# Optimization experiments

Hardware: AMD Instinct MI355X
Metric: run time of the kernel (lower is better)

Reference implementation:

```python
import jax, jax.numpy as jnp
import numpy as np

T, B, I, H = 512, 256, 512, 512


def setup_inputs() -> dict:
    key = jax.random.key(0)
    ks = jax.random.split(key, 10)
    inp = {
        "x": jax.random.normal(ks[0], (T, B, I), dtype=jnp.float32),
        "lengths": jax.random.randint(ks[1], (B,), 1, T + 1).astype(jnp.int64),
        # LSTMCell params, gate order [i, f, g, o]; forget-gate bias init to 1
        "W_ih": jax.random.normal(ks[2], (4 * H, I), dtype=jnp.float32) / np.sqrt(I),
        "W_hh": jax.random.normal(ks[3], (4 * H, H), dtype=jnp.float32) / np.sqrt(H),
        "b_ih": jnp.zeros((4 * H,), jnp.float32).at[H:2 * H].set(1.0),
        "b_hh": jnp.zeros((4 * H,), jnp.float32),
        # multiplicative projections
        "mx_w": jax.random.normal(ks[4], (H, I), dtype=jnp.float32) / np.sqrt(I),
        "mx_b": jnp.zeros((H,), jnp.float32),
        "mh_w": jax.random.normal(ks[5], (H, H), dtype=jnp.float32) / np.sqrt(H),
        "mh_b": jnp.zeros((H,), jnp.float32),
        "h0": jnp.zeros((H,), jnp.float32),
        "c0": jnp.zeros((H,), jnp.float32),
    }
    return inp


def _mlstm(x, lengths, W_ih, W_hh, b_ih, b_hh, mx_w, mx_b, mh_w, mh_b, h0, c0):
    Tn, Bn, _ = x.shape
    Hn = h0.shape[0]
    # Precompute all input-side projections in two big GEMMs (batched over T*B).
    xg = jnp.einsum('tbi,gi->tbg', x, W_ih) + b_ih          # [T,B,4H]
    xm = jnp.einsum('tbi,hi->tbh', x, mx_w) + mx_b          # [T,B,H]
    # active[t,b] = t < lengths[b]; padded steps freeze (h,c) -> packed semantics
    active = (jnp.arange(Tn)[:, None] < lengths[None, :])[..., None]  # [T,B,1]

    def step(carry, inp):
        h, c = carry
        xg_t, xm_t, act = inp
        m = xm_t * (h @ mh_w.T + mh_b)                       # multiplicative hidden
        gates = xg_t + m @ W_hh.T + b_hh                     # cell(x, (m, c))
        i, f, g, o = jnp.split(gates, 4, axis=-1)
        c_new = jax.nn.sigmoid(f) * c + jax.nn.sigmoid(i) * jnp.tanh(g)
        h_new = jax.nn.sigmoid(o) * jnp.tanh(c_new)
        h = jnp.where(act, h_new, h)
        c = jnp.where(act, c_new, c)
        return (h, c), None

    h_init = jnp.broadcast_to(h0, (Bn, Hn))
    c_init = jnp.broadcast_to(c0, (Bn, Hn))
    (h, c), _ = jax.lax.scan(step, (h_init, c_init), (xg, xm, active))
    # Torch code returns final cell state of each sequence, in batch order.
    return c


def reference(x, lengths, W_ih, W_hh, b_ih, b_hh, mx_w, mx_b, mh_w, mh_b, h0, c0):
    return _mlstm(x, lengths, W_ih, W_hh, b_ih, b_hh, mx_w, mx_b, mh_w, mh_b, h0, c0)
```

## Files before the change

kernel.cpp:

```cpp
#include <hip/hip_runtime.h>
#include <stdint.h>


typedef __attribute__((ext_vector_type(8))) short s8v;
typedef __attribute__((ext_vector_type(8))) _Float16 h8v;
typedef __attribute__((ext_vector_type(4))) float f4v;

#define SC 2048.0f
#define ISC (1.0f / 2048.0f)

__device__ __forceinline__ f4v mf(s8v a, s8v b, f4v c) {
  return __builtin_amdgcn_mfma_f32_16x16x32_f16(
      __builtin_bit_cast(h8v, a), __builtin_bit_cast(h8v, b), c, 0, 0, 0);
}
__device__ __forceinline__ uint16_t f2h(float x) {
  _Float16 h = (_Float16)x;
  return __builtin_bit_cast(uint16_t, h);
}
__device__ __forceinline__ void split2(float v, uint16_t& hi, uint16_t& lo) {
  _Float16 h = (_Float16)v;
  float r = v - (float)h;
  hi = __builtin_bit_cast(uint16_t, h);
  lo = f2h(r * SC);
}
__device__ __forceinline__ float sigm(float x) { return 1.0f / (1.0f + __expf(-x)); }
__device__ __forceinline__ float tanh_f(float x) { return 1.0f - 2.0f / (__expf(2.0f * x) + 1.0f); }

__device__ __forceinline__ s8v ldx4_sc1(const uint16_t* p) {
  s8v r;
  asm volatile("global_load_dwordx4 %0, %1, off sc1" : "=v"(r) : "v"(p));
  return r;
}
__device__ __forceinline__ uint32_t ld32_sc1(const uint32_t* p) {
  uint32_t r;
  asm volatile("global_load_dword %0, %1, off sc1" : "=v"(r) : "v"(p));
  return r;
}
__device__ __forceinline__ void st16_sc1(uint16_t* p, uint32_t v) {
  asm volatile("global_store_short %0, %1, off sc1" ::"v"(p), "v"(v) : "memory");
}
__device__ __forceinline__ void st32_sc1(uint32_t* p, uint32_t v) {
  asm volatile("global_store_dword %0, %1, off sc1" ::"v"(p), "v"(v) : "memory");
}

__global__ __launch_bounds__(256) void k_split(const float* __restrict__ x,
                                               uint16_t* __restrict__ xh,
                                               uint16_t* __restrict__ xl, long n) {
  long i = ((long)blockIdx.x * 256 + threadIdx.x) * 8;
  if (i >= n) return;
  float4 a = *(const float4*)(x + i);
  float4 b = *(const float4*)(x + i + 4);
  union { uint16_t u[8]; s8v v; } oh, ol;
  float vv[8] = {a.x, a.y, a.z, a.w, b.x, b.y, b.z, b.w};
#pragma unroll
  for (int k = 0; k < 8; ++k) split2(vv[k], oh.u[k], ol.u[k]);
  *(s8v*)(xh + i) = oh.v;
  *(s8v*)(xl + i) = ol.v;
}

__global__ __launch_bounds__(64) void k_packw(const float* __restrict__ Wg,
                                              const float* __restrict__ Wm,
                                              uint16_t* __restrict__ wh,
                                              uint16_t* __restrict__ wl) {
  int s = blockIdx.x >> 4, kt = blockIdx.x & 15, l = threadIdx.x;
  const float* src = (s < 128) ? (Wg + (size_t)(s * 16 + (l & 15)) * 512)
                               : (Wm + (size_t)((s - 128) * 16 + (l & 15)) * 512);
  int k0 = kt * 32 + (l >> 4) * 8;
  float4 a = *(const float4*)(src + k0);
  float4 b = *(const float4*)(src + k0 + 4);
  union { uint16_t u[8]; s8v v; } oh, ol;
  float vv[8] = {a.x, a.y, a.z, a.w, b.x, b.y, b.z, b.w};
#pragma unroll
  for (int k = 0; k < 8; ++k) split2(vv[k], oh.u[k], ol.u[k]);
  size_t adr = ((size_t)(s * 16 + kt) * 64 + l) * 8;
  *(s8v*)(wh + adr) = oh.v;
  *(s8v*)(wl + adr) = ol.v;
}

__device__ __forceinline__ void gpass(const uint16_t* __restrict__ Ap,
                                      const uint16_t* __restrict__ Bp,
                                      s8v* Asm, s8v* Bsm, int rowbase, int s0,
                                      f4v (&acc)[4][4]) {
  int tid = threadIdx.x;
  int wv = tid >> 6, l = tid & 63, wm = wv >> 1, wn = wv & 1;
  int arow = tid >> 1, ahalf = tid & 1, swz = (arow & 7) << 4;
  for (int ks = 0; ks < 8; ++ks) {
    __syncthreads();
    const uint16_t* asrc = Ap + (size_t)(rowbase + arow) * 512 + ks * 64;
#pragma unroll
    for (int q = 0; q < 4; ++q) {
      int pb = ahalf * 64 + q * 16;
      Asm[arow * 8 + (pb >> 4)] = *(const s8v*)(asrc + ((pb ^ swz) >> 1));
    }
#pragma unroll
    for (int q = 0; q < 4; ++q) {
      int ofs = tid * 64 + q * 16;
      int si = ofs >> 11, kti = (ofs >> 10) & 1, inner = ofs & 1023;
      Bsm[ofs >> 4] =
          *(const s8v*)(Bp + (size_t)((s0 + si) * 16 + ks * 2 + kti) * 512 + (inner >> 1));
    }
    __syncthreads();
#pragma unroll
    for (int kti = 0; kti < 2; ++kti) {
      s8v a[4], b[4];
#pragma unroll
      for (int i = 0; i < 4; ++i) {
        int row = wm * 64 + i * 16 + (l & 15);
        int lb = kti * 64 + (l >> 4) * 16;
        a[i] = Asm[row * 8 + ((lb ^ ((l & 7) << 4)) >> 4)];
      }
#pragma unroll
      for (int jj = 0; jj < 4; ++jj) b[jj] = Bsm[((wn * 4 + jj) * 2 + kti) * 64 + l];
#pragma unroll
      for (int i = 0; i < 4; ++i)
#pragma unroll
        for (int jj = 0; jj < 4; ++jj) acc[i][jj] = mf(a[i], b[jj], acc[i][jj]);
    }
  }
}

__global__ __launch_bounds__(256, 2) void k_gemm3(const uint16_t* __restrict__ xh,
                                                  const uint16_t* __restrict__ xl,
                                                  const uint16_t* __restrict__ wh,
                                                  const uint16_t* __restrict__ wl,
                                                  float* __restrict__ blob, int row0) {
  __shared__ s8v Asm[1024], Bsm[1024];
  f4v acc_a[4][4], acc_c[4][4];
#pragma unroll
  for (int i = 0; i < 4; ++i)
#pragma unroll
    for (int jj = 0; jj < 4; ++jj) {
      acc_a[i][jj] = (f4v){0.f, 0.f, 0.f, 0.f};
      acc_c[i][jj] = (f4v){0.f, 0.f, 0.f, 0.f};
    }
  int s0 = blockIdx.x * 8, r0 = blockIdx.y * 128;
  int rowbase = row0 + r0;
  gpass(xh, wh, Asm, Bsm, rowbase, s0, acc_a);
  gpass(xh, wl, Asm, Bsm, rowbase, s0, acc_c);
  gpass(xl, wh, Asm, Bsm, rowbase, s0, acc_c);
  int tid = threadIdx.x, wv = tid >> 6, l = tid & 63, wm = wv >> 1, wn = wv & 1;
#pragma unroll
  for (int i = 0; i < 4; ++i)
#pragma unroll
    for (int jj = 0; jj < 4; ++jj) {
      int s = s0 + wn * 4 + jj;
#pragma unroll
      for (int ri = 0; ri < 4; ++ri) {
        int trow = r0 + wm * 64 + i * 16 + (l >> 4) * 4 + ri;
        int tt = trow >> 8, gg = (trow >> 5) & 7, rr = trow & 31;
        size_t adr = ((size_t)(tt * 160 + s) * 8 + gg) * 512 + rr * 16 + (l & 15);
        blob[adr] = acc_a[i][jj][ri] + acc_c[i][jj][ri] * ISC;
      }
    }
}

__device__ __forceinline__ void gbar(uint32_t* slots, int myslot, uint32_t ep) {
  asm volatile("s_waitcnt vmcnt(0)" ::: "memory");
  __syncthreads();
  int tid = threadIdx.x;
  if (tid == 0) st32_sc1(slots + myslot, ep);
  if (tid < 64) {
    uint32_t v;
    const uint32_t* q = slots + (tid & 31);
    do {
      __builtin_amdgcn_s_sleep(1);
      v = ld32_sc1(q);
      asm volatile("s_waitcnt vmcnt(0)" ::: "memory");
      __builtin_amdgcn_sched_barrier(0);
    } while (!__all(v >= ep));
  }
  __syncthreads();
}

__global__ __launch_bounds__(128, 1) void k_rec(
    const uint16_t* __restrict__ wrh, const uint16_t* __restrict__ wrl,
    const float* __restrict__ blob,
    const float* __restrict__ b_ih, const float* __restrict__ b_hh,
    const float* __restrict__ mx_b, const float* __restrict__ mh_b,
    const float* __restrict__ h0, const float* __restrict__ c0,
    const int* __restrict__ lengths,
    uint16_t* hh, uint16_t* hl, uint16_t* mhp, uint16_t* mlp,
    float* cbuf, uint32_t* flags, float* out, int chunk) {
  extern __shared__ char smraw[];
  s8v* SW = (s8v*)smraw;
  int tid = threadIdx.x, l = tid & 63, mt = tid >> 6;
  int g = blockIdx.x & 7, j = blockIdx.x >> 3;

  for (int p = 0; p < 2; ++p) {
    const uint16_t* wp = p ? wrl : wrh;
    for (int nt = 0; nt < 4; ++nt) {
      const s8v* src = (const s8v*)(wp + (size_t)(nt * 32 + j) * 8192);
#pragma unroll
      for (int it = 0; it < 8; ++it) SW[p * 4096 + nt * 1024 + it * 128 + tid] = src[it * 128 + tid];
    }
  }
  s8v wmh[16], wml[16];
  {
    const s8v* sH = (const s8v*)(wrh + (size_t)(128 + j) * 8192);
    const s8v* sL = (const s8v*)(wrl + (size_t)(128 + j) * 8192);
#pragma unroll
    for (int kt = 0; kt < 16; ++kt) { wmh[kt] = sH[kt * 64 + l]; wml[kt] = sL[kt * 64 + l]; }
  }
  int cidx = l & 15, rq = l >> 4;
  int hc = j * 16 + cidx;
  float mhb = mh_b[hc], mxb = mx_b[hc];
  float bsum[4];
#pragma unroll
  for (int nt = 0; nt < 4; ++nt) bsum[nt] = b_ih[nt * 512 + hc] + b_hh[nt * 512 + hc];
  int rowA = g * 32 + mt * 16 + cidx;
  int kofs = rq * 8;
  int rowC0 = g * 32 + mt * 16 + rq * 4;
  float creg[4];
  int lenr[4];
#pragma unroll
  for (int ri = 0; ri < 4; ++ri) {
    int r = rowC0 + ri;
    lenr[ri] = lengths[r];
    creg[ri] = (chunk == 0) ? c0[hc] : cbuf[(size_t)r * 512 + hc];
  }
  if (chunk == 0) {
    uint16_t hi, lo;
    split2(h0[hc], hi, lo);
#pragma unroll
    for (int ri = 0; ri < 4; ++ri) {
      st16_sc1(hh + (size_t)(rowC0 + ri) * 512 + hc, hi);
      st16_sc1(hl + (size_t)(rowC0 + ri) * 512 + hc, lo);
    }
  }
  uint32_t* slots = flags + g * 64;
  uint32_t ep = 1;
  gbar(slots, j, ep);

  const uint16_t* hrb = hh + (size_t)rowA * 512 + kofs;
  const uint16_t* lrb = hl + (size_t)rowA * 512 + kofs;
  const uint16_t* mrb = mhp + (size_t)rowA * 512 + kofs;
  const uint16_t* nrb = mlp + (size_t)rowA * 512 + kofs;

  for (int t = 0; t < 128; ++t) {
    size_t bb = ((size_t)(t * 160 + j) * 8 + g) * 512 + (size_t)(mt * 16 + rq * 4) * 16 + cidx;
    float bxm[4], bg[4][4];
#pragma unroll
    for (int ri = 0; ri < 4; ++ri) {
      bxm[ri] = blob[bb + 524288 + ri * 16];
#pragma unroll
      for (int nt = 0; nt < 4; ++nt) bg[nt][ri] = blob[bb + nt * 131072 + ri * 16];
    }
    s8v ah[16], al[16];
#pragma unroll
    for (int kt = 0; kt < 16; ++kt) {
      ah[kt] = ldx4_sc1(hrb + kt * 32);
      al[kt] = ldx4_sc1(lrb + kt * 32);
    }
    asm volatile("s_waitcnt vmcnt(0)" ::: "memory");
    __builtin_amdgcn_sched_barrier(0);
    f4v a1a0 = (f4v){0,0,0,0}, a1a1 = (f4v){0,0,0,0}, a1c0 = (f4v){0,0,0,0}, a1c1 = (f4v){0,0,0,0};
#pragma unroll
    for (int kt = 0; kt < 16; kt += 2) {
      a1a0 = mf(ah[kt], wmh[kt], a1a0);
      a1a1 = mf(ah[kt + 1], wmh[kt + 1], a1a1);
    }
#pragma unroll
    for (int kt = 0; kt < 16; ++kt) {
      a1c0 = mf(ah[kt], wml[kt], a1c0);
      a1c1 = mf(al[kt], wmh[kt], a1c1);
    }
#pragma unroll
    for (int ri = 0; ri < 4; ++ri) {
      float hv = a1a0[ri] + a1a1[ri] + (a1c0[ri] + a1c1[ri]) * ISC + mhb;
      float mv = (bxm[ri] + mxb) * hv;
      uint16_t hi, lo;
      split2(mv, hi, lo);
      st16_sc1(mhp + (size_t)(rowC0 + ri) * 512 + hc, hi);
      st16_sc1(mlp + (size_t)(rowC0 + ri) * 512 + hc, lo);
    }
    ++ep;
    gbar(slots, j, ep);
#pragma unroll
    for (int kt = 0; kt < 16; ++kt) {
      ah[kt] = ldx4_sc1(mrb + kt * 32);
      al[kt] = ldx4_sc1(nrb + kt * 32);
    }
    asm volatile("s_waitcnt vmcnt(0)" ::: "memory");
    __builtin_amdgcn_sched_barrier(0);
    f4v p2a[4], p2c[4];
#pragma unroll
    for (int nt = 0; nt < 4; ++nt) { p2a[nt] = (f4v){0,0,0,0}; p2c[nt] = (f4v){0,0,0,0}; }
#pragma unroll
    for (int kt = 0; kt < 16; ++kt)
#pragma unroll
      for (int nt = 0; nt < 4; ++nt) p2a[nt] = mf(ah[kt], SW[nt * 1024 + kt * 64 + l], p2a[nt]);
#pragma unroll
    for (int kt = 0; kt < 16; ++kt)
#pragma unroll
      for (int nt = 0; nt < 4; ++nt) {
        p2c[nt] = mf(ah[kt], SW[4096 + nt * 1024 + kt * 64 + l], p2c[nt]);
        p2c[nt] = mf(al[kt], SW[nt * 1024 + kt * 64 + l], p2c[nt]);
      }
#pragma unroll
    for (int ri = 0; ri < 4; ++ri) {
      float gi = p2a[0][ri] + p2c[0][ri] * ISC + bsum[0] + bg[0][ri];
      float gf = p2a[1][ri] + p2c[1][ri] * ISC + bsum[1] + bg[1][ri];
      float gc = p2a[2][ri] + p2c[2][ri] * ISC + bsum[2] + bg[2][ri];
      float go = p2a[3][ri] + p2c[3][ri] * ISC + bsum[3] + bg[3][ri];
      float iv = sigm(gi), fv = sigm(gf), gv = tanh_f(gc), ov = sigm(go);
      float cn = fv * creg[ri] + iv * gv;
      float hn = ov * tanh_f(cn);
      bool act = (chunk * 128 + t) < lenr[ri];
      if (act) {
        creg[ri] = cn;
        uint16_t hi, lo;
        split2(hn, hi, lo);
        st16_sc1(hh + (size_t)(rowC0 + ri) * 512 + hc, hi);
        st16_sc1(hl + (size_t)(rowC0 + ri) * 512 + hc, lo);
      }
    }
    ++ep;
    gbar(slots, j, ep);
  }
#pragma unroll
  for (int ri = 0; ri < 4; ++ri) {
    cbuf[(size_t)(rowC0 + ri) * 512 + hc] = creg[ri];
    if (chunk == 3) out[(size_t)(rowC0 + ri) * 512 + hc] = creg[ri];
  }
}

extern "C" void kernel_launch(void* const* d_in, const int* in_sizes, int n_in,
                              void* d_out, int out_size, void* d_ws, size_t ws_size,
                              hipStream_t stream) {
  (void)in_sizes; (void)n_in; (void)out_size;
  const float* x = (const float*)d_in[0];
  const int* lengths = (const int*)d_in[1];
  const float* W_ih = (const float*)d_in[2];
  const float* W_hh = (const float*)d_in[3];
  const float* b_ih = (const float*)d_in[4];
  const float* b_hh = (const float*)d_in[5];
  const float* mx_w = (const float*)d_in[6];
  const float* mx_b = (const float*)d_in[7];
  const float* mh_w = (const float*)d_in[8];
  const float* mh_b = (const float*)d_in[9];
  const float* h0 = (const float*)d_in[10];
  const float* c0 = (const float*)d_in[11];

  if (ws_size < 616040448ull) return;

  char* ws = (char*)d_ws;
  uint16_t* xh = (uint16_t*)(ws);
  uint16_t* xl = (uint16_t*)(ws + 134217728ull);
  uint16_t* wpre_h = (uint16_t*)(ws + 268435456ull);
  uint16_t* wpre_l = (uint16_t*)(ws + 271056896ull);
  uint16_t* wrec_h = (uint16_t*)(ws + 273678336ull);
  uint16_t* wrec_l = (uint16_t*)(ws + 276299776ull);
  float* blob = (float*)(ws + 278921216ull);
  uint16_t* hh = (uint16_t*)(ws + 614465536ull);
  uint16_t* hl = (uint16_t*)(ws + 614727680ull);
  uint16_t* mhp = (uint16_t*)(ws + 614989824ull);
  uint16_t* mlp = (uint16_t*)(ws + 615251968ull);
  float* cbuf = (float*)(ws + 615514112ull);
  uint32_t* flags = (uint32_t*)(ws + 616038400ull);

  k_split<<<32768, 256, 0, stream>>>(x, xh, xl, 67108864L);
  k_packw<<<2560, 64, 0, stream>>>(W_ih, mx_w, wpre_h, wpre_l);
  k_packw<<<2560, 64, 0, stream>>>(W_hh, mh_w, wrec_h, wrec_l);
  hipFuncSetAttribute(reinterpret_cast<const void*>(k_rec),
                      hipFuncAttributeMaxDynamicSharedMemorySize, 131072);
  for (int c = 0; c < 4; ++c) {
    k_gemm3<<<dim3(20, 256), 256, 0, stream>>>(xh, xl, wpre_h, wpre_l, blob, c * 32768);
    hipMemsetAsync(flags, 0, 2048, stream);
    k_rec<<<256, 128, 131072, stream>>>(wrec_h, wrec_l, blob, b_ih, b_hh, mx_b, mh_b,
                                        h0, c0, lengths, hh, hl, mhp, mlp, cbuf,
                                        flags, (float*)d_out, c);
  }
}
```

Measured before the change: 8.768 ms.

## Replace block-wide grid barriers with per-wave flag polling over 16-row groups

Each wave now owns a 16-row batch group and synchronises only with the 32 waves sharing that group through separate m and h flag arrays, instead of a block-wide __syncthreads plus 32-slot barrier. The blob layout is reindexed to the finer 16-row grouping, and the h-ready flag is published at the end of a step but polled only after the next step's blob loads, letting those loads overlap the wait. Register pressure is cut by moving the low mh weights into LDS, which grows shared memory to 144 KiB, and by loading high and low activation fragments in sequence. The cost is more flag traffic and serialised load-then-MFMA phases with extra vmcnt waits.

After: 8.448 ms. -3.6%, faster.

```diff
diff --git a/kernel.cpp b/kernel.cpp
--- a/kernel.cpp
+++ b/kernel.cpp
@@ -42,6 +42,11 @@
 __device__ __forceinline__ void st32_sc1(uint32_t* p, uint32_t v) {
   asm volatile("global_store_dword %0, %1, off sc1" ::"v"(p), "v"(v) : "memory");
 }
+#define VM0                                              \
+  do {                                                   \
+    asm volatile("s_waitcnt vmcnt(0)" ::: "memory");     \
+    __builtin_amdgcn_sched_barrier(0);                   \
+  } while (0)
 
 __global__ __launch_bounds__(256) void k_split(const float* __restrict__ x,
                                                uint16_t* __restrict__ xh,
@@ -147,29 +152,21 @@
 #pragma unroll
       for (int ri = 0; ri < 4; ++ri) {
         int trow = r0 + wm * 64 + i * 16 + (l >> 4) * 4 + ri;
-        int tt = trow >> 8, gg = (trow >> 5) & 7, rr = trow & 31;
-        size_t adr = ((size_t)(tt * 160 + s) * 8 + gg) * 512 + rr * 16 + (l & 15);
+        int tt = trow >> 8, gg = (trow >> 4) & 15, rr = trow & 15;
+        size_t adr = ((size_t)(tt * 160 + s) * 16 + gg) * 256 + rr * 16 + (l & 15);
         blob[adr] = acc_a[i][jj][ri] + acc_c[i][jj][ri] * ISC;
       }
     }
 }
 
-__device__ __forceinline__ void gbar(uint32_t* slots, int myslot, uint32_t ep) {
-  asm volatile("s_waitcnt vmcnt(0)" ::: "memory");
-  __syncthreads();
-  int tid = threadIdx.x;
-  if (tid == 0) st32_sc1(slots + myslot, ep);
-  if (tid < 64) {
-    uint32_t v;
-    const uint32_t* q = slots + (tid & 31);
-    do {
-      __builtin_amdgcn_s_sleep(1);
-      v = ld32_sc1(q);
-      asm volatile("s_waitcnt vmcnt(0)" ::: "memory");
-      __builtin_amdgcn_sched_barrier(0);
-    } while (!__all(v >= ep));
-  }
-  __syncthreads();
+__device__ __forceinline__ void spoll(const uint32_t* slots, uint32_t ep, int l) {
+  const uint32_t* q = slots + (l & 31);
+  for (;;) {
+    uint32_t v = ld32_sc1(q);
+    VM0;
+    if (__all((int)(v >= ep))) break;
+    __builtin_amdgcn_s_sleep(1);
+  }
 }
 
 __global__ __launch_bounds__(128, 1) void k_rec(
@@ -183,33 +180,33 @@
     float* cbuf, uint32_t* flags, float* out, int chunk) {
   extern __shared__ char smraw[];
   s8v* SW = (s8v*)smraw;
-  int tid = threadIdx.x, l = tid & 63, mt = tid >> 6;
-  int g = blockIdx.x & 7, j = blockIdx.x >> 3;
-
-  for (int p = 0; p < 2; ++p) {
-    const uint16_t* wp = p ? wrl : wrh;
-    for (int nt = 0; nt < 4; ++nt) {
-      const s8v* src = (const s8v*)(wp + (size_t)(nt * 32 + j) * 8192);
-#pragma unroll
-      for (int it = 0; it < 8; ++it) SW[p * 4096 + nt * 1024 + it * 128 + tid] = src[it * 128 + tid];
-    }
-  }
-  s8v wmh[16], wml[16];
+  int tid = threadIdx.x, l = tid & 63, wv = tid >> 6;
+  int j = blockIdx.x >> 3, gg = ((blockIdx.x & 7) << 1) | wv;
+
+#pragma unroll
+  for (int sl = 0; sl < 9; ++sl) {
+    int gs = (sl < 4) ? (sl * 32 + j) : (sl < 8 ? (sl - 4) * 32 + j : 128 + j);
+    const s8v* src = (const s8v*)(((sl < 4) ? wrh : wrl) + (size_t)gs * 8192);
+#pragma unroll
+    for (int it = 0; it < 8; ++it) SW[sl * 1024 + it * 128 + tid] = src[it * 128 + tid];
+  }
+  s8v wmh[16];
   {
     const s8v* sH = (const s8v*)(wrh + (size_t)(128 + j) * 8192);
-    const s8v* sL = (const s8v*)(wrl + (size_t)(128 + j) * 8192);
-#pragma unroll
-    for (int kt = 0; kt < 16; ++kt) { wmh[kt] = sH[kt * 64 + l]; wml[kt] = sL[kt * 64 + l]; }
-  }
+#pragma unroll
+    for (int kt = 0; kt < 16; ++kt) wmh[kt] = sH[kt * 64 + l];
+  }
+  __syncthreads();
+
   int cidx = l & 15, rq = l >> 4;
   int hc = j * 16 + cidx;
   float mhb = mh_b[hc], mxb = mx_b[hc];
   float bsum[4];
 #pragma unroll
   for (int nt = 0; nt < 4; ++nt) bsum[nt] = b_ih[nt * 512 + hc] + b_hh[nt * 512 + hc];
-  int rowA = g * 32 + mt * 16 + cidx;
+  int rowA = gg * 16 + cidx;
   int kofs = rq * 8;
-  int rowC0 = g * 32 + mt * 16 + rq * 4;
+  int rowC0 = gg * 16 + rq * 4;
   float creg[4];
   int lenr[4];
 #pragma unroll
@@ -218,6 +215,9 @@
     lenr[ri] = lengths[r];
     creg[ri] = (chunk == 0) ? c0[hc] : cbuf[(size_t)r * 512 + hc];
   }
+  uint32_t* mslot = flags + gg * 32;
+  uint32_t* hslot = flags + 512 + gg * 32;
+
   if (chunk == 0) {
     uint16_t hi, lo;
     split2(h0[hc], hi, lo);
@@ -227,9 +227,9 @@
       st16_sc1(hl + (size_t)(rowC0 + ri) * 512 + hc, lo);
     }
   }
-  uint32_t* slots = flags + g * 64;
-  uint32_t ep = 1;
-  gbar(slots, j, ep);
+  asm volatile("s_waitcnt vmcnt(0)" ::: "memory");
+  if (l == 0) st32_sc1(hslot + j, 1u);
+  spoll(hslot, 1u, l);
 
   const uint16_t* hrb = hh + (size_t)rowA * 512 + kofs;
   const uint16_t* lrb = hl + (size_t)rowA * 512 + kofs;
@@ -237,33 +237,34 @@
   const uint16_t* nrb = mlp + (size_t)rowA * 512 + kofs;
 
   for (int t = 0; t < 128; ++t) {
-    size_t bb = ((size_t)(t * 160 + j) * 8 + g) * 512 + (size_t)(mt * 16 + rq * 4) * 16 + cidx;
+    size_t tb = ((size_t)(t * 160) * 16 + (size_t)gg) * 256 + rq * 64 + cidx;
     float bxm[4], bg[4][4];
 #pragma unroll
     for (int ri = 0; ri < 4; ++ri) {
-      bxm[ri] = blob[bb + 524288 + ri * 16];
-#pragma unroll
-      for (int nt = 0; nt < 4; ++nt) bg[nt][ri] = blob[bb + nt * 131072 + ri * 16];
-    }
-    s8v ah[16], al[16];
-#pragma unroll
-    for (int kt = 0; kt < 16; ++kt) {
-      ah[kt] = ldx4_sc1(hrb + kt * 32);
-      al[kt] = ldx4_sc1(lrb + kt * 32);
-    }
-    asm volatile("s_waitcnt vmcnt(0)" ::: "memory");
-    __builtin_amdgcn_sched_barrier(0);
-    f4v a1a0 = (f4v){0,0,0,0}, a1a1 = (f4v){0,0,0,0}, a1c0 = (f4v){0,0,0,0}, a1c1 = (f4v){0,0,0,0};
+      bxm[ri] = blob[tb + (size_t)(128 + j) * 4096 + ri * 16];
+#pragma unroll
+      for (int nt = 0; nt < 4; ++nt)
+        bg[nt][ri] = blob[tb + (size_t)(nt * 32 + j) * 4096 + ri * 16];
+    }
+    if (t > 0) spoll(hslot, (uint32_t)(t + 1), l);
+    s8v af[16];
+#pragma unroll
+    for (int kt = 0; kt < 16; ++kt) af[kt] = ldx4_sc1(hrb + kt * 32);
+    VM0;
+    f4v a1a0 = (f4v){0,0,0,0}, a1a1 = (f4v){0,0,0,0};
+    f4v a1c0 = (f4v){0,0,0,0}, a1c1 = (f4v){0,0,0,0};
 #pragma unroll
     for (int kt = 0; kt < 16; kt += 2) {
-      a1a0 = mf(ah[kt], wmh[kt], a1a0);
-      a1a1 = mf(ah[kt + 1], wmh[kt + 1], a1a1);
-    }
-#pragma unroll
-    for (int kt = 0; kt < 16; ++kt) {
-      a1c0 = mf(ah[kt], wml[kt], a1c0);
-      a1c1 = mf(al[kt], wmh[kt], a1c1);
-    }
+      a1a0 = mf(af[kt], wmh[kt], a1a0);
+      a1a1 = mf(af[kt + 1], wmh[kt + 1], a1a1);
+    }
+#pragma unroll
+    for (int kt = 0; kt < 16; ++kt) a1c0 = mf(af[kt], SW[8 * 1024 + kt * 64 + l], a1c0);
+#pragma unroll
+    for (int kt = 0; kt < 16; ++kt) af[kt] = ldx4_sc1(lrb + kt * 32);
+    VM0;
+#pragma unroll
+    for (int kt = 0; kt < 16; ++kt) a1c1 = mf(af[kt], wmh[kt], a1c1);
 #pragma unroll
     for (int ri = 0; ri < 4; ++ri) {
       float hv = a1a0[ri] + a1a1[ri] + (a1c0[ri] + a1c1[ri]) * ISC + mhb;
@@ -273,35 +274,39 @@
       st16_sc1(mhp + (size_t)(rowC0 + ri) * 512 + hc, hi);
       st16_sc1(mlp + (size_t)(rowC0 + ri) * 512 + hc, lo);
     }
-    ++ep;
-    gbar(slots, j, ep);
-#pragma unroll
-    for (int kt = 0; kt < 16; ++kt) {
-      ah[kt] = ldx4_sc1(mrb + kt * 32);
-      al[kt] = ldx4_sc1(nrb + kt * 32);
-    }
     asm volatile("s_waitcnt vmcnt(0)" ::: "memory");
-    __builtin_amdgcn_sched_barrier(0);
-    f4v p2a[4], p2c[4];
-#pragma unroll
-    for (int nt = 0; nt < 4; ++nt) { p2a[nt] = (f4v){0,0,0,0}; p2c[nt] = (f4v){0,0,0,0}; }
+    if (l == 0) st32_sc1(mslot + j, (uint32_t)(t + 1));
+    spoll(mslot, (uint32_t)(t + 1), l);
+    f4v p2a[4], p2c[4], p2d[4];
+#pragma unroll
+    for (int nt = 0; nt < 4; ++nt) {
+      p2a[nt] = (f4v){0,0,0,0};
+      p2c[nt] = (f4v){0,0,0,0};
+      p2d[nt] = (f4v){0,0,0,0};
+    }
+#pragma unroll
+    for (int kt = 0; kt < 16; ++kt) af[kt] = ldx4_sc1(mrb + kt * 32);
+    VM0;
 #pragma unroll
     for (int kt = 0; kt < 16; ++kt)
 #pragma unroll
-      for (int nt = 0; nt < 4; ++nt) p2a[nt] = mf(ah[kt], SW[nt * 1024 + kt * 64 + l], p2a[nt]);
+      for (int nt = 0; nt < 4; ++nt) {
+        p2a[nt] = mf(af[kt], SW[nt * 1024 + kt * 64 + l], p2a[nt]);
+        p2c[nt] = mf(af[kt], SW[(4 + nt) * 1024 + kt * 64 + l], p2c[nt]);
+      }
+#pragma unroll
+    for (int kt = 0; kt < 16; ++kt) af[kt] = ldx4_sc1(nrb + kt * 32);
+    VM0;
 #pragma unroll
     for (int kt = 0; kt < 16; ++kt)
 #pragma unroll
-      for (int nt = 0; nt < 4; ++nt) {
-        p2c[nt] = mf(ah[kt], SW[4096 + nt * 1024 + kt * 64 + l], p2c[nt]);
-        p2c[nt] = mf(al[kt], SW[nt * 1024 + kt * 64 + l], p2c[nt]);
-      }
+      for (int nt = 0; nt < 4; ++nt) p2d[nt] = mf(af[kt], SW[nt * 1024 + kt * 64 + l], p2d[nt]);
 #pragma unroll
     for (int ri = 0; ri < 4; ++ri) {
-      float gi = p2a[0][ri] + p2c[0][ri] * ISC + bsum[0] + bg[0][ri];
-      float gf = p2a[1][ri] + p2c[1][ri] * ISC + bsum[1] + bg[1][ri];
-      float gc = p2a[2][ri] + p2c[2][ri] * ISC + bsum[2] + bg[2][ri];
-      float go = p2a[3][ri] + p2c[3][ri] * ISC + bsum[3] + bg[3][ri];
+      float gi = p2a[0][ri] + (p2c[0][ri] + p2d[0][ri]) * ISC + bsum[0] + bg[0][ri];
+      float gf = p2a[1][ri] + (p2c[1][ri] + p2d[1][ri]) * ISC + bsum[1] + bg[1][ri];
+      float gc = p2a[2][ri] + (p2c[2][ri] + p2d[2][ri]) * ISC + bsum[2] + bg[2][ri];
+      float go = p2a[3][ri] + (p2c[3][ri] + p2d[3][ri]) * ISC + bsum[3] + bg[3][ri];
       float iv = sigm(gi), fv = sigm(gf), gv = tanh_f(gc), ov = sigm(go);
       float cn = fv * creg[ri] + iv * gv;
       float hn = ov * tanh_f(cn);
@@ -314,8 +319,10 @@
         st16_sc1(hl + (size_t)(rowC0 + ri) * 512 + hc, lo);
       }
     }
-    ++ep;
-    gbar(slots, j, ep);
+    if (t < 127) {
+      asm volatile("s_waitcnt vmcnt(0)" ::: "memory");
+      if (l == 0) st32_sc1(hslot + j, (uint32_t)(t + 2));
+    }
   }
 #pragma unroll
   for (int ri = 0; ri < 4; ++ri) {
@@ -341,7 +348,7 @@
   const float* h0 = (const float*)d_in[10];
   const float* c0 = (const float*)d_in[11];
 
-  if (ws_size < 616040448ull) return;
+  if (ws_size < 616042496ull) return;
 
   char* ws = (char*)d_ws;
   uint16_t* xh = (uint16_t*)(ws);
@@ -362,11 +369,11 @@
   k_packw<<<2560, 64, 0, stream>>>(W_ih, mx_w, wpre_h, wpre_l);
   k_packw<<<2560, 64, 0, stream>>>(W_hh, mh_w, wrec_h, wrec_l);
   hipFuncSetAttribute(reinterpret_cast<const void*>(k_rec),
-                      hipFuncAttributeMaxDynamicSharedMemorySize, 131072);
+                      hipFuncAttributeMaxDynamicSharedMemorySize, 147456);
   for (int c = 0; c < 4; ++c) {
     k_gemm3<<<dim3(20, 256), 256, 0, stream>>>(xh, xl, wpre_h, wpre_l, blob, c * 32768);
-    hipMemsetAsync(flags, 0, 2048, stream);
-    k_rec<<<256, 128, 131072, stream>>>(wrec_h, wrec_l, blob, b_ih, b_hh, mx_b, mh_b,
+    hipMemsetAsync(flags, 0, 4096, stream);
+    k_rec<<<256, 128, 147456, stream>>>(wrec_h, wrec_l, blob, b_ih, b_hh, mx_b, mh_b,
                                         h0, c0, lengths, hh, hl, mhp, mlp, cbuf,
                                         flags, (float*)d_out, c);
   }
```
